# Kernel tuning notes

Measured on AMD Instinct MI355X. Metric: run time of the kernel, lower is better.

Reference implementation:

```python
import jax, jax.numpy as jnp
import numpy as np

N = 50000
E = 800000
IN_DIM = 128
HID = 64
HEADS = 4

def _gat_layer(h, src, dst, W, al, ar, Wres, activation):
    # h: [N, F_in]; W: [F_in, HEADS*HID]; al/ar: [HEADS, HID]
    n = h.shape[0]
    ft = (h @ W).reshape(n, HEADS, HID)                    # [N,H,D]
    el = (ft * al).sum(-1)                                  # [N,H]
    er = (ft * ar).sum(-1)                                  # [N,H]
    e = jax.nn.leaky_relu(el[src] + er[dst], 0.2)           # [E,H]
    m = jax.ops.segment_max(e, dst, num_segments=n)         # per-dst max for stable softmax
    ex = jnp.exp(e - m[dst])
    den = jax.ops.segment_sum(ex, dst, num_segments=n)
    alpha = ex / den[dst]                                   # edge softmax [E,H]
    out = jax.ops.segment_sum(alpha[:, :, None] * ft[src], dst, num_segments=n)  # [N,H,D]
    res = (h @ Wres).reshape(n, HEADS, HID) if Wres is not None else h.reshape(n, HEADS, HID)
    out = out + res
    return activation(out) if activation is not None else out


def setup_inputs() -> dict:
    key = jax.random.key(0)
    ks = jax.random.split(key, 16)
    def lin(k, fi, fo):
        return jax.random.normal(k, (fi, fo), jnp.float32) / np.sqrt(fi)
    HD = HEADS * HID
    inp = {
        "h": jax.random.normal(ks[0], (N, IN_DIM), jnp.float32),
        "src": jax.random.randint(ks[1], (E,), 0, N, jnp.int32),
        "dst": jax.random.randint(ks[2], (E,), 0, N, jnp.int32),
        "W1": lin(ks[3], IN_DIM, HD),
        "Wr1": lin(ks[4], IN_DIM, HD),
        "al1": jax.random.normal(ks[5], (HEADS, HID), jnp.float32) * 0.1,
        "ar1": jax.random.normal(ks[6], (HEADS, HID), jnp.float32) * 0.1,
        "W2": lin(ks[7], HD, HD),
        "al2": jax.random.normal(ks[8], (HEADS, HID), jnp.float32) * 0.1,
        "ar2": jax.random.normal(ks[9], (HEADS, HID), jnp.float32) * 0.1,
        "W3": lin(ks[10], HD, HD),
        "al3": jax.random.normal(ks[11], (HEADS, HID), jnp.float32) * 0.1,
        "ar3": jax.random.normal(ks[12], (HEADS, HID), jnp.float32) * 0.1,
        "Wm1": lin(ks[13], HID, HID),
        "bm1": jnp.zeros((HID,), jnp.float32),
        "Wm2": lin(ks[14], HID, 1),
        "bm2": jnp.zeros((1,), jnp.float32),
    }
    return inp


def reference(h, src, dst, W1, Wr1, al1, ar1, W2, al2, ar2, W3, al3, ar3, Wm1, bm1, Wm2, bm2):
    x = _gat_layer(h, src, dst, W1, al1, ar1, Wr1, jax.nn.relu)   # [N,H,D]
    x = x.reshape(x.shape[0], -1)                                  # [N,H*D]
    x = _gat_layer(x, src, dst, W2, al2, ar2, None, jax.nn.relu)  # identity residual (in==H*D)
    x = x.reshape(x.shape[0], -1)
    x = _gat_layer(x, src, dst, W3, al3, ar3, None, None)
    hf = x.mean(1)                                                 # [N,HID]
    diff = jnp.abs(hf[src] - hf[dst])                              # [E,HID]
    z = jax.nn.relu(diff @ Wm1 + bm1)
    score = jax.nn.sigmoid(z @ Wm2 + bm2).squeeze(-1)              # [E]
    return score
```

## Files before the change

kernel.cpp:

```cpp
#include <hip/hip_runtime.h>
#include <hip/hip_bf16.h>

typedef unsigned short u16;
typedef unsigned char u8;
typedef __attribute__((ext_vector_type(8))) short bf16x8;
typedef __attribute__((ext_vector_type(4))) float f32x4;
typedef __attribute__((ext_vector_type(2))) float f32x2;

__device__ __forceinline__ float bf2f(u16 u){
  union { unsigned int i; float f; } v; v.i = ((unsigned int)u) << 16; return v.f;
}
__device__ __forceinline__ u16 f2bf(float f){
  union { float f; unsigned int i; } v; v.f = f;
  unsigned int lsb = (v.i >> 16) & 1u;
  v.i += 0x7fffu + lsb;
  return (u16)(v.i >> 16);
}
__device__ __forceinline__ unsigned pkbf(float a, float b){
  __hip_bfloat162 h = __float22bfloat162_rn(make_float2(a, b));
  union { __hip_bfloat162 h2; unsigned u; } c; c.h2 = h; return c.u;
}
__device__ __forceinline__ u8 f2fp8(float f){
  int p = __builtin_amdgcn_cvt_pk_fp8_f32(f, f, 0, false);
  return (u8)(p & 0xFF);
}

__global__ void k_sniff(const u16* __restrict__ p, int* __restrict__ flag){
  __shared__ int s[256];
  int tid = threadIdx.x;
  u16 v = p[2 * tid];
  int e = (v >> 7) & 0xFF;
  s[tid] = (e >= 100 && e <= 135) ? 1 : 0;
  __syncthreads();
  for (int off = 128; off; off >>= 1){
    if (tid < off) s[tid] += s[tid + off];
    __syncthreads();
  }
  if (tid == 0) *flag = (s[0] < 180) ? 1 : 0;
}

struct PrepEnt { const void* s; void* d; void* d2; int n; int K; int mode; int bstart; };
struct Prep16 { PrepEnt e[16]; };
__global__ void k_prep(Prep16 tab, const u16* __restrict__ hsrc){
  __shared__ int s[256];
  __shared__ u16 tl[32][33];
  {
    int tid = threadIdx.x;
    u16 v = hsrc[2 * tid];
    int e = (v >> 7) & 0xFF;
    s[tid] = (e >= 100 && e <= 135) ? 1 : 0;
    __syncthreads();
    for (int off = 128; off; off >>= 1){
      if (tid < off) s[tid] += s[tid + off];
      __syncthreads();
    }
  }
  const int flag = (s[0] < 180) ? 1 : 0;
  __syncthreads();

  const int bx = blockIdx.x;
  int y = 0;
  #pragma unroll
  for (int i = 1; i < 16; ++i) if (bx >= tab.e[i].bstart) y = i;
  PrepEnt en = tab.e[y];
  const int nblk = ((y < 15) ? tab.e[y + 1].bstart : (int)gridDim.x) - en.bstart;
  const int lb = bx - en.bstart;
  const int T = nblk * 256;
  const int t0 = lb * 256 + threadIdx.x;

  if (en.mode == 1){
    u16* d = (u16*)en.d;
    for (int i = t0; i < en.n; i += T){
      u16 o[4];
      if (flag){
        float4 v = ((const float4*)en.s)[i];
        o[0] = f2bf(v.x); o[1] = f2bf(v.y); o[2] = f2bf(v.z); o[3] = f2bf(v.w);
      } else {
        uint2 v = ((const uint2*)en.s)[i];
        o[0] = (u16)v.x; o[1] = (u16)(v.x >> 16); o[2] = (u16)v.y; o[3] = (u16)(v.y >> 16);
      }
      uint2 w; w.x = o[0] | ((unsigned)o[1] << 16); w.y = o[2] | ((unsigned)o[3] << 16);
      ((uint2*)d)[i] = w;
    }
  } else if (en.mode == 0){
    u16* d = (u16*)en.d;
    for (int i = t0; i < en.n; i += T){
      if (flag) d[i] = f2bf(((const float*)en.s)[i]);
      else      d[i] = ((const u16*)en.s)[i];
    }
  } else if (en.mode == 2){
    u16* wt = (u16*)en.d;
    const int K = en.K;
    const int tk = lb >> 3, tc = lb & 7;
    const int tx = threadIdx.x & 31, ty = threadIdx.x >> 5;
    #pragma unroll
    for (int r = 0; r < 4; ++r){
      int row = tk * 32 + ty + r * 8, col = tc * 32 + tx;
      u16 b;
      if (flag) b = f2bf(((const float*)en.s)[row * 256 + col]);
      else      b = ((const u16*)en.s)[row * 256 + col];
      tl[ty + r * 8][tx] = b;
    }
    __syncthreads();
    #pragma unroll
    for (int r = 0; r < 4; ++r){
      int c = tc * 32 + ty + r * 8, k = tk * 32 + tx;
      wt[(size_t)c * K + k] = tl[tx][ty + r * 8];
    }
  }
}

__global__ void k_scan1(int4* __restrict__ cnt4, int* __restrict__ rowptr,
                        int* __restrict__ bsums, int N){
  __shared__ int s[256];
  int i = blockIdx.x * 256 + threadIdx.x;
  int4 c = make_int4(0, 0, 0, 0);
  if (i < N) c = cnt4[i];
  int v = c.x + c.y + c.z + c.w;
  if (i < N) cnt4[i] = make_int4(0, c.x, c.x + c.y, c.x + c.y + c.z);
  s[threadIdx.x] = v; __syncthreads();
  for (int off = 1; off < 256; off <<= 1){
    int x = 0;
    if (threadIdx.x >= off) x = s[threadIdx.x - off];
    __syncthreads();
    s[threadIdx.x] += x;
    __syncthreads();
  }
  if (i < N) rowptr[i + 1] = s[threadIdx.x];
  if (threadIdx.x == 255) bsums[blockIdx.x] = s[255];
}
__global__ void k_scan2(int* __restrict__ bsums, int nb){
  __shared__ int s[256];
  int t = threadIdx.x;
  int v = (t < nb) ? bsums[t] : 0;
  s[t] = v; __syncthreads();
  for (int off = 1; off < 256; off <<= 1){
    int x = 0;
    if (t >= off) x = s[t - off];
    __syncthreads();
    s[t] += x;
    __syncthreads();
  }
  if (t < nb) bsums[t] = s[t] - v;
}
__global__ void k_scan3(int* __restrict__ rowptr, const int* __restrict__ bsums, int N){
  int i = blockIdx.x * 256 + threadIdx.x;
  if (i < N){
    rowptr[i + 1] += bsums[blockIdx.x];
    if (i == 0) rowptr[0] = 0;
  }
}
__global__ void k_place(const int* __restrict__ src, const int* __restrict__ dst,
                        const int* __restrict__ slot, const int* __restrict__ rowptr,
                        const int* __restrict__ cur4, int4* __restrict__ csrp, int E){
  const int T = gridDim.x * 256;
  for (int i = blockIdx.x * 256 + threadIdx.x; i < E; i += T){
    int d = dst[i];
    int base = cur4[(d << 2) | (i & 3)];
    csrp[rowptr[d] + base + slot[i]] = make_int4(src[i], d, i, 0);
  }
}
__global__ void k_extract(const int4* __restrict__ csrp, int* __restrict__ csrs, int E){
  int i = blockIdx.x * 256 + threadIdx.x;
  if (i < E) csrs[i] = csrp[i].x;
}

#define GWAIT8() asm volatile("s_waitcnt vmcnt(8)" ::: "memory")
#define GWAIT0() asm volatile("s_waitcnt vmcnt(0)" ::: "memory")
#define GBAR()   do { __builtin_amdgcn_s_barrier(); __builtin_amdgcn_sched_barrier(0); } while (0)

__global__ __launch_bounds__(256, 4) void mfma_gemm_v6(
    const u16* __restrict__ X, const u16* __restrict__ WT, const u16* __restrict__ WTr,
    u8* __restrict__ FT8, u16* __restrict__ XA,
    const u16* __restrict__ al, const u16* __restrict__ ar,
    float* __restrict__ el4, float* __restrict__ er4, int N, int K,
    const int* __restrict__ edst, int* __restrict__ slotp, int* __restrict__ cur4,
    int Etot, int do_csr)
{
  extern __shared__ u16 Bs[];
  const int wv = threadIdx.x >> 6;
  const int lane = threadIdx.x & 63;
  const int m = lane & 15;
  const int q = lane >> 4;
  const int mh = m & 7;
  const int row0 = blockIdx.x * 128 + wv * 32;
  const int col0 = blockIdx.y * 128;
  const u16* W = (blockIdx.z == 0) ? WT : WTr;

  f32x4 acc[2][8];
  #pragma unroll
  for (int g = 0; g < 2; ++g)
    #pragma unroll
    for (int t = 0; t < 8; ++t) acc[g][t] = (f32x4){0.f, 0.f, 0.f, 0.f};
  const int rA = row0 + m, rB = row0 + 16 + m;
  const bool vA = rA < N, vB = rB < N;
  const u16* apA = X + (size_t)rA * K + q * 8;
  const u16* apB = X + (size_t)rB * K + q * 8;

  auto stageC = [&](int c, int buf){
    u16* base = Bs + buf * 8192;
    const u16* Wk = W + c * 64;
    #pragma unroll
    for (int j = 0; j < 4; ++j){
      int cbase = (j * 4 + wv) * 64;
      int ci = cbase + lane;
      int col = ci >> 3, slot = ci & 7;
      int gslot = slot ^ (col & 7);
      const u16* srcp = Wk + (size_t)(col0 + col) * K + gslot * 8;
      __builtin_amdgcn_global_load_lds((const unsigned int*)srcp,
                                       (unsigned int*)(base + cbase * 8), 16, 0, 0);
    }
  };
  auto loadA = [&](int c, bf16x8* a){
    const int kb = c * 64;
    bf16x8 z = {};
    a[0] = z; a[1] = z; a[2] = z; a[3] = z;
    if (vA){ a[0] = *(const bf16x8*)(apA + kb); a[2] = *(const bf16x8*)(apA + kb + 32); }
    if (vB){ a[1] = *(const bf16x8*)(apB + kb); a[3] = *(const bf16x8*)(apB + kb + 32); }
  };
  auto compute = [&](const u16* __restrict__ Bb, const bf16x8* a){
    #pragma unroll
    for (int ks = 0; ks < 2; ++ks){
      const int sb = ks * 4 + q;
      #pragma unroll
      for (int t = 0; t < 8; ++t){
        const u16* bp = Bb + (size_t)(t * 16 + m) * 64 + (size_t)(sb ^ mh) * 8;
        bf16x8 b = *(const bf16x8*)bp;
        acc[0][t] = __builtin_amdgcn_mfma_f32_16x16x32_bf16(a[2 * ks],     b, acc[0][t], 0, 0, 0);
        acc[1][t] = __builtin_amdgcn_mfma_f32_16x16x32_bf16(a[2 * ks + 1], b, acc[1][t], 0, 0, 0);
      }
    }
  };

  const int nc = K >> 6;
  bf16x8 a0[4], a1[4];
  stageC(0, 0);
  loadA(0, a0);
  for (int c = 0; c < nc; c += 2){
    if (c + 1 < nc){ stageC(c + 1, 1); loadA(c + 1, a1); GWAIT8(); }
    else           { GWAIT0(); }
    GBAR();
    compute(Bs, a0);
    GBAR();
    if (c + 1 < nc){
      if (c + 2 < nc){ stageC(c + 2, 0); loadA(c + 2, a0); GWAIT8(); }
      else           { GWAIT0(); }
      GBAR();
      compute(Bs + 8192, a1);
      GBAR();
    }
  }

  int ce0 = 0, ce1 = 0, cp0 = 0, cp1 = 0;
  bool cb0 = false, cb1 = false;
  if (do_csr){
    const int nbk = gridDim.x * 4;
    const int bid = ((blockIdx.z * 2 + blockIdx.y) * gridDim.x) + blockIdx.x;
    const int epb = (Etot + nbk - 1) / nbk;
    const int elo = bid * epb;
    const int ehi = min(elo + epb, Etot);
    ce0 = elo + (int)threadIdx.x;
    ce1 = ce0 + 256;
    cb0 = ce0 < ehi; cb1 = ce1 < ehi;
    int d0 = 0, d1 = 0;
    if (cb0) d0 = edst[ce0];
    if (cb1) d1 = edst[ce1];
    if (cb0) cp0 = atomicAdd(&cur4[(d0 << 2) | (ce0 & 3)], 1);
    if (cb1) cp1 = atomicAdd(&cur4[(d1 << 2) | (ce1 & 3)], 1);
    for (int e = elo + (int)threadIdx.x + 512; e < ehi; e += 256){
      int dd = edst[e];
      slotp[e] = atomicAdd(&cur4[(dd << 2) | (e & 3)], 1);
    }
  }

  if (blockIdx.z == 0){
    float alv[8], arv[8];
    #pragma unroll
    for (int t = 0; t < 8; ++t){
      alv[t] = bf2f(al[col0 + t * 16 + m]);
      arv[t] = bf2f(ar[col0 + t * 16 + m]);
    }
    #pragma unroll
    for (int g = 0; g < 2; ++g)
      #pragma unroll
      for (int r = 0; r < 4; ++r){
        float pe[2] = {0.f, 0.f}, pr[2] = {0.f, 0.f};
        #pragma unroll
        for (int t = 0; t < 8; ++t){
          pe[t >> 2] += acc[g][t][r] * alv[t];
          pr[t >> 2] += acc[g][t][r] * arv[t];
        }
        #pragma unroll
        for (int mk = 1; mk < 16; mk <<= 1){
          pe[0] += __shfl_xor(pe[0], mk); pe[1] += __shfl_xor(pe[1], mk);
          pr[0] += __shfl_xor(pr[0], mk); pr[1] += __shfl_xor(pr[1], mk);
        }
        int rr = row0 + g * 16 + q * 4 + r;
        if (m == 0 && rr < N){
          *(float2*)(el4 + (size_t)rr * 4 + blockIdx.y * 2) = make_float2(pe[0], pe[1]);
          *(float2*)(er4 + (size_t)rr * 4 + blockIdx.y * 2) = make_float2(pr[0], pr[1]);
        }
      }
    #pragma unroll
    for (int g = 0; g < 2; ++g)
      #pragma unroll
      for (int t = 0; t < 8; ++t){
        int col = col0 + t * 16 + m;
        #pragma unroll
        for (int r = 0; r < 4; ++r){
          int rr = row0 + g * 16 + q * 4 + r;
          if (rr < N) FT8[(size_t)rr * 256 + col] = f2fp8(acc[g][t][r]);
        }
      }
  } else {
    #pragma unroll
    for (int g = 0; g < 2; ++g)
      #pragma unroll
      for (int t = 0; t < 8; ++t){
        int col = col0 + t * 16 + m;
        #pragma unroll
        for (int r = 0; r < 4; ++r){
          int rr = row0 + g * 16 + q * 4 + r;
          if (rr < N) XA[(size_t)rr * 256 + col] = f2bf(acc[g][t][r]);
        }
      }
  }

  if (do_csr){
    if (cb0) slotp[ce0] = cp0;
    if (cb1) slotp[ce1] = cp1;
  }
}

__global__ __launch_bounds__(256) void aggregate8(
    const u8* __restrict__ ft8, const float* __restrict__ el4, const float* __restrict__ er4,
    const int* __restrict__ rowptr, const int* __restrict__ csrs,
    const u16* __restrict__ residb, u16* __restrict__ outb,
    u16* __restrict__ hf, int do_hf, int N)
{
  __shared__ float sal[4][4][17][4];
  __shared__ int   sof[4][4][16];
  const int w = threadIdx.x >> 6, lane = threadIdx.x & 63;
  const int g = lane >> 4, t = lane & 15;
  const int hd = t >> 2;
  const int d = blockIdx.x * 16 + w * 4 + g;
  const bool vd = d < N;
  int beg = 0, deg = 0;
  if (vd){ beg = rowptr[d]; deg = rowptr[d + 1] - beg; }
  int mdeg = deg;
  mdeg = max(mdeg, __shfl_xor(mdeg, 16));
  mdeg = max(mdeg, __shfl_xor(mdeg, 32));
  float4 erd = make_float4(0.f, 0.f, 0.f, 0.f);
  if (vd) erd = ((const float4*)er4)[d];

  f32x2 acc2[8];
  #pragma unroll
  for (int i = 0; i < 8; ++i) acc2[i] = (f32x2){0.f, 0.f};
  float den[4] = {0.f, 0.f, 0.f, 0.f};

  for (int c0 = 0; c0 < mdeg; c0 += 16){
    const int rem = deg - c0;
    float t0 = 0.f, t1 = 0.f, t2 = 0.f, t3 = 0.f; int s = 0;
    if (t < rem){
      s = csrs[beg + c0 + t];
      float4 ql = ((const float4*)el4)[s];
      float e0 = ql.x + erd.x; e0 = (e0 > 0.f) ? e0 : 0.2f * e0;
      float e1 = ql.y + erd.y; e1 = (e1 > 0.f) ? e1 : 0.2f * e1;
      float e2 = ql.z + erd.z; e2 = (e2 > 0.f) ? e2 : 0.2f * e2;
      float e3 = ql.w + erd.w; e3 = (e3 > 0.f) ? e3 : 0.2f * e3;
      t0 = __expf(fminf(e0, 60.f)); t1 = __expf(fminf(e1, 60.f));
      t2 = __expf(fminf(e2, 60.f)); t3 = __expf(fminf(e3, 60.f));
    }
    den[0] += t0; den[1] += t1; den[2] += t2; den[3] += t3;
    sal[w][g][t][0] = t0; sal[w][g][t][1] = t1;
    sal[w][g][t][2] = t2; sal[w][g][t][3] = t3;
    sof[w][g][t] = s << 8;
    __builtin_amdgcn_wave_barrier();
    int cr = rem < 16 ? (rem < 0 ? 0 : rem) : 16;
    int jm = (cr + 3) & ~3;
    for (int j = 0; j < jm; j += 4){
      float a[4]; unsigned off[4]; uint4 v[4];
      #pragma unroll
      for (int u = 0; u < 4; ++u){
        a[u] = sal[w][g][j + u][hd];
        off[u] = (unsigned)sof[w][g][j + u];
      }
      #pragma unroll
      for (int u = 0; u < 4; ++u)
        v[u] = *(const uint4*)(ft8 + (size_t)off[u] + t * 16);
      #pragma unroll
      for (int u = 0; u < 4; ++u){
        f32x2 a2 = (f32x2){a[u], a[u]};
        acc2[0] += __builtin_amdgcn_cvt_pk_f32_fp8(v[u].x, 0) * a2;
        acc2[1] += __builtin_amdgcn_cvt_pk_f32_fp8(v[u].x, 1) * a2;
        acc2[2] += __builtin_amdgcn_cvt_pk_f32_fp8(v[u].y, 0) * a2;
        acc2[3] += __builtin_amdgcn_cvt_pk_f32_fp8(v[u].y, 1) * a2;
        acc2[4] += __builtin_amdgcn_cvt_pk_f32_fp8(v[u].z, 0) * a2;
        acc2[5] += __builtin_amdgcn_cvt_pk_f32_fp8(v[u].z, 1) * a2;
        acc2[6] += __builtin_amdgcn_cvt_pk_f32_fp8(v[u].w, 0) * a2;
        acc2[7] += __builtin_amdgcn_cvt_pk_f32_fp8(v[u].w, 1) * a2;
      }
    }
    __builtin_amdgcn_wave_barrier();
  }
  #pragma unroll
  for (int mk = 1; mk < 16; mk <<= 1){
    den[0] += __shfl_xor(den[0], mk); den[1] += __shfl_xor(den[1], mk);
    den[2] += __shfl_xor(den[2], mk); den[3] += __shfl_xor(den[3], mk);
  }
  const float dh = den[hd];
  const float inv = (dh > 0.f) ? (1.f / dh) : 0.f;

  if (!vd) return;
  const u16* rp = residb + (size_t)d * 256 + t * 16;
  uint4 r0 = *(const uint4*)rp;
  uint4 r1 = *(const uint4*)(rp + 8);
  float o[16];
  {
    union { unsigned u; float f; } x;
    unsigned rw[8] = {r0.x, r0.y, r0.z, r0.w, r1.x, r1.y, r1.z, r1.w};
    #pragma unroll
    for (int i = 0; i < 8; ++i){
      x.u = rw[i] << 16;          o[2 * i]     = x.f;
      x.u = rw[i] & 0xffff0000u;  o[2 * i + 1] = x.f;
    }
  }
  #pragma unroll
  for (int i = 0; i < 8; ++i){
    o[2 * i]     += acc2[i].x * inv;
    o[2 * i + 1] += acc2[i].y * inv;
  }
  if (!do_hf){
    uint4 a, b;
    a.x = pkbf(fmaxf(o[0], 0.f),  fmaxf(o[1], 0.f));
    a.y = pkbf(fmaxf(o[2], 0.f),  fmaxf(o[3], 0.f));
    a.z = pkbf(fmaxf(o[4], 0.f),  fmaxf(o[5], 0.f));
    a.w = pkbf(fmaxf(o[6], 0.f),  fmaxf(o[7], 0.f));
    b.x = pkbf(fmaxf(o[8], 0.f),  fmaxf(o[9], 0.f));
    b.y = pkbf(fmaxf(o[10], 0.f), fmaxf(o[11], 0.f));
    b.z = pkbf(fmaxf(o[12], 0.f), fmaxf(o[13], 0.f));
    b.w = pkbf(fmaxf(o[14], 0.f), fmaxf(o[15], 0.f));
    u16* op = outb + (size_t)d * 256 + t * 16;
    *(uint4*)op = a;
    *(uint4*)(op + 8) = b;
  } else {
    #pragma unroll
    for (int i = 0; i < 16; ++i){
      float v = o[i];
      v += __shfl_xor(v, 4);
      v += __shfl_xor(v, 8);
      o[i] = 0.25f * v;
    }
    if (t < 4){
      uint4 a, b;
      a.x = pkbf(o[0], o[1]);   a.y = pkbf(o[2], o[3]);
      a.z = pkbf(o[4], o[5]);   a.w = pkbf(o[6], o[7]);
      b.x = pkbf(o[8], o[9]);   b.y = pkbf(o[10], o[11]);
      b.z = pkbf(o[12], o[13]); b.w = pkbf(o[14], o[15]);
      u16* hp = hf + (size_t)d * 64 + t * 16;
      *(uint4*)hp = a;
      *(uint4*)(hp + 8) = b;
    }
  }
}

__global__ __launch_bounds__(256) void edge_mlp_csr(
    const u16* __restrict__ hfb, const int4* __restrict__ csrp,
    const u16* __restrict__ Wm1, const u16* __restrict__ bm1,
    const u16* __restrict__ Wm2, const u16* __restrict__ bm2,
    void* __restrict__ out, int E, const int* __restrict__ flag)
{
  const int lane = threadIdx.x & 63;
  const int m = lane & 15;
  const int q = lane >> 4;
  const int is_f32 = *flag;

  bf16x8 bfr[4][2];
  #pragma unroll
  for (int t = 0; t < 4; ++t)
    #pragma unroll
    for (int ks = 0; ks < 2; ++ks)
      #pragma unroll
      for (int j = 0; j < 8; ++j)
        bfr[t][ks][j] = (short)Wm1[(size_t)(ks * 32 + q * 8 + j) * 64 + t * 16 + m];

  float b1v[4], w2v[4];
  #pragma unroll
  for (int t = 0; t < 4; ++t){
    b1v[t] = bf2f(bm1[t * 16 + m]);
    w2v[t] = bf2f(Wm2[t * 16 + m]);
  }
  const float b2 = bf2f(bm2[0]);

  const int wid = blockIdx.x * 4 + (threadIdx.x >> 6);
  const int nw  = gridDim.x * 4;
  for (int e0 = wid * 16; e0 < E; e0 += nw * 16){
    int e = e0 + m; if (e >= E) e = E - 1;
    int4 ed = csrp[e];
    const u16* ps = hfb + (size_t)ed.x * 64;
    const u16* pd = hfb + (size_t)ed.y * 64;
    union { bf16x8 v; uint4 u; } af[2];
    #pragma unroll
    for (int ks = 0; ks < 2; ++ks){
      bf16x8 vs = *(const bf16x8*)(ps + ks * 32 + q * 8);
      bf16x8 vd = *(const bf16x8*)(pd + ks * 32 + q * 8);
      unsigned pk[4];
      #pragma unroll
      for (int pp = 0; pp < 4; ++pp){
        float a0 = fabsf(bf2f((u16)vs[2 * pp])     - bf2f((u16)vd[2 * pp]));
        float a1 = fabsf(bf2f((u16)vs[2 * pp + 1]) - bf2f((u16)vd[2 * pp + 1]));
        pk[pp] = pkbf(a0, a1);
      }
      af[ks].u = make_uint4(pk[0], pk[1], pk[2], pk[3]);
    }
    f32x4 acc[4];
    #pragma unroll
    for (int t = 0; t < 4; ++t) acc[t] = (f32x4){0.f, 0.f, 0.f, 0.f};
    #pragma unroll
    for (int ks = 0; ks < 2; ++ks)
      #pragma unroll
      for (int t = 0; t < 4; ++t)
        acc[t] = __builtin_amdgcn_mfma_f32_16x16x32_bf16(af[ks].v, bfr[t][ks], acc[t], 0, 0, 0);
    #pragma unroll
    for (int r = 0; r < 4; ++r){
      float p = 0.f;
      #pragma unroll
      for (int t = 0; t < 4; ++t)
        p += fmaxf(acc[t][r] + b1v[t], 0.f) * w2v[t];
      #pragma unroll
      for (int mm = 1; mm < 16; mm <<= 1) p += __shfl_xor(p, mm);
      int slot = e0 + q * 4 + r;
      if (m == 0 && slot < E){
        int eid = csrp[slot].z;
        float sc = 1.f / (1.f + __expf(-(p + b2)));
        if (is_f32) ((float*)out)[eid] = sc;
        else        ((u16*)out)[eid]   = f2bf(sc);
      }
    }
  }
}

extern "C" void kernel_launch(void* const* d_in, const int* in_sizes, int n_in,
                              void* d_out, int out_size, void* d_ws, size_t ws_size,
                              hipStream_t stream)
{
  const int* src = (const int*)d_in[1];
  const int* dst = (const int*)d_in[2];

  const int N = in_sizes[0] / 128;
  const int E = in_sizes[1];

  char* p = (char*)d_ws;
  auto alloc = [&](size_t bytes) -> char* {
    char* r = p; p += (bytes + 255) & ~(size_t)255; return r;
  };
  int* flag   = (int*)  alloc(4);
  u16* hc     = (u16*)  alloc((size_t)N * 128 * 2);
  u8*  FT8    = (u8*)   alloc((size_t)N * 256);
  u16* XA     = (u16*)  alloc((size_t)N * 256 * 2);
  u16* XB     = (u16*)  alloc((size_t)N * 256 * 2);
  float* el   = (float*)alloc((size_t)N * 4 * 4);
  float* er   = (float*)alloc((size_t)N * 4 * 4);
  u16* hfb    = (u16*)  alloc((size_t)N * 64 * 2);
  int* rowptr = (int*)  alloc((size_t)(N + 1) * 4);
  int* cur4   = (int*)  alloc((size_t)N * 16);
  int* slot   = (int*)  alloc((size_t)E * 4);
  int4* csrp  = (int4*) alloc((size_t)E * 16);
  int* csrs   = (int*)  alloc((size_t)E * 4);
  int* bsums  = (int*)  alloc(1024);
  u16* WT1    = (u16*)  alloc(128 * 256 * 2);
  u16* WTr1   = (u16*)  alloc(128 * 256 * 2);
  u16* WT2    = (u16*)  alloc(256 * 256 * 2);
  u16* WT3    = (u16*)  alloc(256 * 256 * 2);
  u16* al1c   = (u16*)  alloc(256 * 2);
  u16* ar1c   = (u16*)  alloc(256 * 2);
  u16* al2c   = (u16*)  alloc(256 * 2);
  u16* ar2c   = (u16*)  alloc(256 * 2);
  u16* al3c   = (u16*)  alloc(256 * 2);
  u16* ar3c   = (u16*)  alloc(256 * 2);
  u16* Wm1c   = (u16*)  alloc(4096 * 2);
  u16* bm1c   = (u16*)  alloc(64 * 2);
  u16* Wm2c   = (u16*)  alloc(64 * 2);
  u16* bm2c   = (u16*)  alloc(2);

  const int nb = (N + 255) / 256;
  const int ge = (E + 255) / 256;
  const u16* hsrc = (const u16*)d_in[0];

  k_sniff<<<1, 256, 0, stream>>>(hsrc, flag);
  hipMemsetAsync(cur4, 0, (size_t)N * 16, stream);

  {
    Prep16 t{};
    int b = 0;
    auto put = [&](int idx, const void* s, void* d, void* d2, int n, int K,
                   int mode, int nblk){
      t.e[idx] = {s, d, d2, n, K, mode, b};
      b += nblk;
    };
    put(0,  d_in[0],  hc,    nullptr, N * 32,   0,   1, 768);
    put(1,  d_in[3],  WT1,   nullptr, 0,        128, 2, 32);
    put(2,  d_in[4],  WTr1,  nullptr, 0,        128, 2, 32);
    put(3,  d_in[7],  WT2,   nullptr, 0,        256, 2, 64);
    put(4,  d_in[10], WT3,   nullptr, 0,        256, 2, 64);
    put(5,  d_in[5],  al1c,  nullptr, 256,      0,   0, 1);
    put(6,  d_in[6],  ar1c,  nullptr, 256,      0,   0, 1);
    put(7,  d_in[8],  al2c,  nullptr, 256,      0,   0, 1);
    put(8,  d_in[9],  ar2c,  nullptr, 256,      0,   0, 1);
    put(9,  d_in[11], al3c,  nullptr, 256,      0,   0, 1);
    put(10, d_in[12], ar3c,  nullptr, 256,      0,   0, 1);
    put(11, d_in[13], Wm1c,  nullptr, 4096,     0,   0, 1);
    put(12, d_in[14], bm1c,  nullptr, 64,       0,   0, 1);
    put(13, d_in[15], Wm2c,  nullptr, 64,       0,   0, 1);
    put(14, d_in[16], bm2c,  nullptr, 1,        0,   0, 1);
    put(15, nullptr,  nullptr, nullptr, 0,      0,   0, 0);
    k_prep<<<dim3(b), 256, 0, stream>>>(t, hsrc);
  }

  const dim3 gA3((N + 127) / 128, 2);
  const dim3 gL1((N + 127) / 128, 2, 2);
  const int gG = (N + 15) / 16;
  const int ldsP = 2 * 128 * 64 * 2;

  mfma_gemm_v6<<<gL1, 256, ldsP, stream>>>(hc, WT1, WTr1, FT8, XA, al1c, ar1c,
                                           el, er, N, 128, dst, slot, cur4, E, 1);
  k_scan1<<<nb, 256, 0, stream>>>((int4*)cur4, rowptr, bsums, N);
  k_scan2<<<1, 256, 0, stream>>>(bsums, nb);
  k_scan3<<<nb, 256, 0, stream>>>(rowptr, bsums, N);
  k_place<<<512, 256, 0, stream>>>(src, dst, slot, rowptr, cur4, csrp, E);
  k_extract<<<ge, 256, 0, stream>>>(csrp, csrs, E);

  aggregate8<<<gG, 256, 0, stream>>>(FT8, el, er, rowptr, csrs, XA, XB, nullptr, 0, N);
  mfma_gemm_v6<<<gA3, 256, ldsP, stream>>>(XB, WT2, WT2, FT8, XA, al2c, ar2c,
                                           el, er, N, 256, nullptr, nullptr, nullptr, 0, 0);
  aggregate8<<<gG, 256, 0, stream>>>(FT8, el, er, rowptr, csrs, XB, XA, nullptr, 0, N);
  mfma_gemm_v6<<<gA3, 256, ldsP, stream>>>(XA, WT3, WT3, FT8, XB, al3c, ar3c,
                                           el, er, N, 256, nullptr, nullptr, nullptr, 0, 0);
  aggregate8<<<gG, 256, 0, stream>>>(FT8, el, er, rowptr, csrs, XA, nullptr, hfb, 1, N);
  edge_mlp_csr<<<2048, 256, 0, stream>>>(hfb, csrp, Wm1c, bm1c, Wm2c, bm2c,
                                         d_out, E, flag);
}
```

Measured before the change: 401.9 us.

## Halve GEMM row tile, swap MFMA operands for row-contiguous packed epilogue stores

The GEMM block tile shrinks from 128 to 64 rows, so each wave computes 16 rows instead of 32. The grid doubles and launch bounds allow more resident blocks. The MFMA operands are swapped so each lane holds four consecutive output columns of one row. That lets the epilogue write packed 4-byte fp8 and 8-byte bf16 stores instead of scattered single-element stores, and reduces the attention-logit dot product with two cross-lane shuffles instead of four. The cost is that each staged weight tile is reused by half as many rows, roughly doubling LDS/weight traffic per output.

```diff
diff --git a/kernel.cpp b/kernel.cpp
--- a/kernel.cpp
+++ b/kernel.cpp
@@ -165,11 +165,11 @@
   if (i < E) csrs[i] = csrp[i].x;
 }
 
-#define GWAIT8() asm volatile("s_waitcnt vmcnt(8)" ::: "memory")
+#define GWAIT6() asm volatile("s_waitcnt vmcnt(6)" ::: "memory")
 #define GWAIT0() asm volatile("s_waitcnt vmcnt(0)" ::: "memory")
 #define GBAR()   do { __builtin_amdgcn_s_barrier(); __builtin_amdgcn_sched_barrier(0); } while (0)
 
-__global__ __launch_bounds__(256, 4) void mfma_gemm_v6(
+__global__ __launch_bounds__(256, 5) void mfma_gemm_v7(
     const u16* __restrict__ X, const u16* __restrict__ WT, const u16* __restrict__ WTr,
     u8* __restrict__ FT8, u16* __restrict__ XA,
     const u16* __restrict__ al, const u16* __restrict__ ar,
@@ -183,19 +183,16 @@
   const int m = lane & 15;
   const int q = lane >> 4;
   const int mh = m & 7;
-  const int row0 = blockIdx.x * 128 + wv * 32;
+  const int row0 = blockIdx.x * 64 + wv * 16;
   const int col0 = blockIdx.y * 128;
   const u16* W = (blockIdx.z == 0) ? WT : WTr;
 
-  f32x4 acc[2][8];
+  f32x4 acc[8];
   #pragma unroll
-  for (int g = 0; g < 2; ++g)
-    #pragma unroll
-    for (int t = 0; t < 8; ++t) acc[g][t] = (f32x4){0.f, 0.f, 0.f, 0.f};
-  const int rA = row0 + m, rB = row0 + 16 + m;
-  const bool vA = rA < N, vB = rB < N;
+  for (int t = 0; t < 8; ++t) acc[t] = (f32x4){0.f, 0.f, 0.f, 0.f};
+  const int rA = row0 + m;
+  const bool vA = rA < N;
   const u16* apA = X + (size_t)rA * K + q * 8;
-  const u16* apB = X + (size_t)rB * K + q * 8;
 
   auto stageC = [&](int c, int buf){
     u16* base = Bs + buf * 8192;
@@ -214,9 +211,8 @@
   auto loadA = [&](int c, bf16x8* a){
     const int kb = c * 64;
     bf16x8 z = {};
-    a[0] = z; a[1] = z; a[2] = z; a[3] = z;
-    if (vA){ a[0] = *(const bf16x8*)(apA + kb); a[2] = *(const bf16x8*)(apA + kb + 32); }
-    if (vB){ a[1] = *(const bf16x8*)(apB + kb); a[3] = *(const bf16x8*)(apB + kb + 32); }
+    a[0] = z; a[1] = z;
+    if (vA){ a[0] = *(const bf16x8*)(apA + kb); a[1] = *(const bf16x8*)(apA + kb + 32); }
   };
   auto compute = [&](const u16* __restrict__ Bb, const bf16x8* a){
     #pragma unroll
@@ -226,24 +222,23 @@
       for (int t = 0; t < 8; ++t){
         const u16* bp = Bb + (size_t)(t * 16 + m) * 64 + (size_t)(sb ^ mh) * 8;
         bf16x8 b = *(const bf16x8*)bp;
-        acc[0][t] = __builtin_amdgcn_mfma_f32_16x16x32_bf16(a[2 * ks],     b, acc[0][t], 0, 0, 0);
-        acc[1][t] = __builtin_amdgcn_mfma_f32_16x16x32_bf16(a[2 * ks + 1], b, acc[1][t], 0, 0, 0);
+        acc[t] = __builtin_amdgcn_mfma_f32_16x16x32_bf16(b, a[ks], acc[t], 0, 0, 0);
       }
     }
   };
 
   const int nc = K >> 6;
-  bf16x8 a0[4], a1[4];
+  bf16x8 a0[2], a1[2];
   stageC(0, 0);
   loadA(0, a0);
   for (int c = 0; c < nc; c += 2){
-    if (c + 1 < nc){ stageC(c + 1, 1); loadA(c + 1, a1); GWAIT8(); }
+    if (c + 1 < nc){ stageC(c + 1, 1); loadA(c + 1, a1); GWAIT6(); }
     else           { GWAIT0(); }
     GBAR();
     compute(Bs, a0);
     GBAR();
     if (c + 1 < nc){
-      if (c + 2 < nc){ stageC(c + 2, 0); loadA(c + 2, a0); GWAIT8(); }
+      if (c + 2 < nc){ stageC(c + 2, 0); loadA(c + 2, a0); GWAIT6(); }
       else           { GWAIT0(); }
       GBAR();
       compute(Bs + 8192, a1);
@@ -274,56 +269,52 @@
   }
 
   if (blockIdx.z == 0){
-    float alv[8], arv[8];
+    uint2 alp[8], arp[8];
     #pragma unroll
     for (int t = 0; t < 8; ++t){
-      alv[t] = bf2f(al[col0 + t * 16 + m]);
-      arv[t] = bf2f(ar[col0 + t * 16 + m]);
-    }
-    #pragma unroll
-    for (int g = 0; g < 2; ++g)
+      alp[t] = *(const uint2*)(al + col0 + t * 16 + q * 4);
+      arp[t] = *(const uint2*)(ar + col0 + t * 16 + q * 4);
+    }
+    auto halv = [](uint2 p, int r) -> float {
+      unsigned w = (r < 2) ? p.x : p.y;
+      return bf2f((u16)((r & 1) ? (w >> 16) : (w & 0xffff)));
+    };
+    float pe[2] = {0.f, 0.f}, pr[2] = {0.f, 0.f};
+    #pragma unroll
+    for (int t = 0; t < 8; ++t)
       #pragma unroll
       for (int r = 0; r < 4; ++r){
-        float pe[2] = {0.f, 0.f}, pr[2] = {0.f, 0.f};
-        #pragma unroll
-        for (int t = 0; t < 8; ++t){
-          pe[t >> 2] += acc[g][t][r] * alv[t];
-          pr[t >> 2] += acc[g][t][r] * arv[t];
-        }
-        #pragma unroll
-        for (int mk = 1; mk < 16; mk <<= 1){
-          pe[0] += __shfl_xor(pe[0], mk); pe[1] += __shfl_xor(pe[1], mk);
-          pr[0] += __shfl_xor(pr[0], mk); pr[1] += __shfl_xor(pr[1], mk);
-        }
-        int rr = row0 + g * 16 + q * 4 + r;
-        if (m == 0 && rr < N){
-          *(float2*)(el4 + (size_t)rr * 4 + blockIdx.y * 2) = make_float2(pe[0], pe[1]);
-          *(float2*)(er4 + (size_t)rr * 4 + blockIdx.y * 2) = make_float2(pr[0], pr[1]);
-        }
-      }
-    #pragma unroll
-    for (int g = 0; g < 2; ++g)
+        pe[t >> 2] += acc[t][r] * halv(alp[t], r);
+        pr[t >> 2] += acc[t][r] * halv(arp[t], r);
+      }
+    pe[0] += __shfl_xor(pe[0], 16); pe[0] += __shfl_xor(pe[0], 32);
+    pe[1] += __shfl_xor(pe[1], 16); pe[1] += __shfl_xor(pe[1], 32);
+    pr[0] += __shfl_xor(pr[0], 16); pr[0] += __shfl_xor(pr[0], 32);
+    pr[1] += __shfl_xor(pr[1], 16); pr[1] += __shfl_xor(pr[1], 32);
+    if (q == 0 && vA){
+      *(float2*)(el4 + (size_t)rA * 4 + blockIdx.y * 2) = make_float2(pe[0], pe[1]);
+      *(float2*)(er4 + (size_t)rA * 4 + blockIdx.y * 2) = make_float2(pr[0], pr[1]);
+    }
+    if (vA){
+      u8* op = FT8 + (size_t)rA * 256 + col0 + q * 4;
       #pragma unroll
       for (int t = 0; t < 8; ++t){
-        int col = col0 + t * 16 + m;
-        #pragma unroll
-        for (int r = 0; r < 4; ++r){
-          int rr = row0 + g * 16 + q * 4 + r;
-          if (rr < N) FT8[(size_t)rr * 256 + col] = f2fp8(acc[g][t][r]);
-        }
-      }
+        int pw = __builtin_amdgcn_cvt_pk_fp8_f32(acc[t][0], acc[t][1], 0, false);
+        pw = __builtin_amdgcn_cvt_pk_fp8_f32(acc[t][2], acc[t][3], pw, true);
+        *(int*)(op + t * 16) = pw;
+      }
+    }
   } else {
-    #pragma unroll
-    for (int g = 0; g < 2; ++g)
+    if (vA){
+      u16* op = XA + (size_t)rA * 256 + col0 + q * 4;
       #pragma unroll
       for (int t = 0; t < 8; ++t){
-        int col = col0 + t * 16 + m;
-        #pragma unroll
-        for (int r = 0; r < 4; ++r){
-          int rr = row0 + g * 16 + q * 4 + r;
-          if (rr < N) XA[(size_t)rr * 256 + col] = f2bf(acc[g][t][r]);
-        }
-      }
+        uint2 w;
+        w.x = pkbf(acc[t][0], acc[t][1]);
+        w.y = pkbf(acc[t][2], acc[t][3]);
+        *(uint2*)(op + t * 16) = w;
+      }
+    }
   }
 
   if (do_csr){
@@ -617,12 +608,12 @@
     k_prep<<<dim3(b), 256, 0, stream>>>(t, hsrc);
   }
 
-  const dim3 gA3((N + 127) / 128, 2);
-  const dim3 gL1((N + 127) / 128, 2, 2);
+  const dim3 gA3((N + 63) / 64, 2);
+  const dim3 gL1((N + 63) / 64, 2, 2);
   const int gG = (N + 15) / 16;
   const int ldsP = 2 * 128 * 64 * 2;
 
-  mfma_gemm_v6<<<gL1, 256, ldsP, stream>>>(hc, WT1, WTr1, FT8, XA, al1c, ar1c,
+  mfma_gemm_v7<<<gL1, 256, ldsP, stream>>>(hc, WT1, WTr1, FT8, XA, al1c, ar1c,
                                            el, er, N, 128, dst, slot, cur4, E, 1);
   k_scan1<<<nb, 256, 0, stream>>>((int4*)cur4, rowptr, bsums, N);
   k_scan2<<<1, 256, 0, stream>>>(bsums, nb);
@@ -631,10 +622,10 @@
   k_extract<<<ge, 256, 0, stream>>>(csrp, csrs, E);
 
   aggregate8<<<gG, 256, 0, stream>>>(FT8, el, er, rowptr, csrs, XA, XB, nullptr, 0, N);
-  mfma_gemm_v6<<<gA3, 256, ldsP, stream>>>(XB, WT2, WT2, FT8, XA, al2c, ar2c,
+  mfma_gemm_v7<<<gA3, 256, ldsP, stream>>>(XB, WT2, WT2, FT8, XA, al2c, ar2c,
                                            el, er, N, 256, nullptr, nullptr, nullptr, 0, 0);
   aggregate8<<<gG, 256, 0, stream>>>(FT8, el, er, rowptr, csrs, XB, XA, nullptr, 0, N);
-  mfma_gemm_v6<<<gA3, 256, ldsP, stream>>>(XA, WT3, WT3, FT8, XB, al3c, ar3c,
+  mfma_gemm_v7<<<gA3, 256, ldsP, stream>>>(XA, WT3, WT3, FT8, XB, al3c, ar3c,
                                            el, er, N, 256, nullptr, nullptr, nullptr, 0, 0);
   aggregate8<<<gG, 256, 0, stream>>>(FT8, el, er, rowptr, csrs, XA, nullptr, hfb, 1, N);
   edge_mlp_csr<<<2048, 256, 0, stream>>>(hfb, csrp, Wm1c, bm1c, Wm2c, bm2c,
```

Measured after the change: 394.9 us. No clear change (-1.7%).
